# Optimization experiments

Hardware: AMD Instinct MI355X
Metric: run time of the kernel (lower is better)

The kernel has to match this reference:

```python
import jax, jax.numpy as jnp
from jax import lax
import numpy as np

GAMMA = 1.0
BIG = 1e10  # stand-in for +inf; exp(-BIG/gamma) underflows to 0 and keeps grads finite


def pairwise_sq_euclidean(A, B):
    # A: (B,T1,K), B: (B,T2,K) -> (B,T1,T2); 0.5*||a-b||^2 expanded to avoid (B,T1,T2,K)
    aa = 0.5 * jnp.sum(A * A, axis=-1)  # (B,T1)
    bb = 0.5 * jnp.sum(B * B, axis=-1)  # (B,T2)
    ab = jnp.einsum('bik,bjk->bij', A, B)
    return aa[:, :, None] + bb[:, None, :] - ab


def soft_dtw(C, gamma):
    # C: (B, m, n). Sequential DP: V[i,j] = C[i-1,j-1] + softmin_gamma(V[i,j-1], V[i-1,j-1], V[i-1,j])
    Bsz, m, n = C.shape
    dt = C.dtype
    big = jnp.asarray(BIG, dt)
    # row 0 of V: V[0,0]=0, V[0,j]=inf
    v0 = jnp.concatenate([jnp.zeros((Bsz, 1), dt), jnp.full((Bsz, n), big, dt)], axis=1)

    def row_step(v_prev, c_row):
        # v_prev: (B, n+1) = V[i-1, :]; c_row: (B, n) = C[:, i-1, :]
        def col_step(v_left, inp):
            c, v_diag, v_up = inp  # each (B,)
            prev = jnp.stack([v_left, v_diag, v_up], axis=-1)  # (B,3)
            minv = -gamma * jax.nn.logsumexp(-prev / gamma, axis=-1)
            v_new = c + minv
            return v_new, v_new

        xs = (c_row.T, v_prev[:, :-1].T, v_prev[:, 1:].T)  # (n, B) each
        _, vals = lax.scan(col_step, jnp.full((Bsz,), big, dt), xs)
        v_row = jnp.concatenate([jnp.full((Bsz, 1), big, dt), vals.T], axis=1)
        return v_row, None

    v_final, _ = lax.scan(row_step, v0, jnp.moveaxis(C, 1, 0))
    return v_final[:, -1]  # (B,)


def setup_inputs() -> dict:
    key = jax.random.key(0)
    k1, k2 = jax.random.split(key)
    X = jax.random.normal(k1, (512, 256, 64), dtype=jnp.float32)
    Y = jax.random.normal(k2, (512, 256, 64), dtype=jnp.float32)
    return {"X": X, "Y": Y}


def reference(X, Y):
    gamma = jnp.asarray(GAMMA, X.dtype)
    s_xy = soft_dtw(pairwise_sq_euclidean(X, Y), gamma)
    s_xx = soft_dtw(pairwise_sq_euclidean(X, X), gamma)
    s_yy = soft_dtw(pairwise_sq_euclidean(Y, Y), gamma)
    D = s_xy - 0.5 * s_xx - 0.5 * s_yy
    # normalize=False, reduction='mean'
    return jnp.mean(D)
```

## Files before the change

### kernel.cpp

```cpp
#include <hip/hip_runtime.h>

typedef float f4 __attribute__((ext_vector_type(4)));

#define BIGV 1e10f
#define LOG2E 1.44269504f
#define LN2 0.69314718f
#define RSTR 66

__device__ __forceinline__ float softmin3b(float a, float b, float c) {
  float m, d, M;
  asm("v_min3_f32 %0, %1, %2, %3" : "=v"(m) : "v"(a), "v"(b), "v"(c));
  asm("v_max3_f32 %0, %1, %2, %3" : "=v"(M) : "v"(a), "v"(b), "v"(c));
  asm("v_med3_f32 %0, %1, %2, %3" : "=v"(d) : "v"(a), "v"(b), "v"(c));
  float s = 1.0f + __builtin_amdgcn_exp2f(m - d) + __builtin_amdgcn_exp2f(m - M);
  return m - __log2f(s);
}

__device__ __forceinline__ float sumsq_fp8x4(unsigned int pk) {
  float d0 = __builtin_amdgcn_cvt_f32_fp8((int)pk, 0);
  float d1 = __builtin_amdgcn_cvt_f32_fp8((int)pk, 1);
  float d2 = __builtin_amdgcn_cvt_f32_fp8((int)pk, 2);
  float d3 = __builtin_amdgcn_cvt_f32_fp8((int)pk, 3);
  return (d0 * d0 + d1 * d1) + (d2 * d2 + d3 * d3);
}

__global__ __launch_bounds__(64)
void sdtw_c(const float* __restrict__ X, const float* __restrict__ Y,
            float* __restrict__ out) {
  const int p = blockIdx.x;
  const int type = p >> 9;
  const int b = p & 511;
  const float* Ap = (type == 2 ? Y : X) + (size_t)b * 256 * 64;
  const float* Bp = (type == 1 ? X : Y) + (size_t)b * 256 * 64;
  const float wgt = (type == 0) ? (LN2 / 512.0f) : (-LN2 / 1024.0f);

  __shared__ unsigned int ring[32 * RSTR];
  __shared__ unsigned int sB[4096];
  __shared__ _Float16 saa[256];
  __shared__ _Float16 sbb[256];

  const int t = threadIdx.x;
  const int hk = t >> 4, lr = t & 15;

  #pragma unroll 1
  for (int i = 0; i < 33; ++i) {
    int idx = i * 64 + t;
    if (idx < 32 * RSTR) ring[idx] = 0u;
  }

  {
    const float4* B4 = (const float4*)Bp;
    const int q = t & 15;
    #pragma unroll 1
    for (int it = 0; it < 64; ++it) {
      int pidx = it * 64 + t;
      int row = pidx >> 4;
      float4 v = B4[pidx];
      unsigned int pk = __builtin_amdgcn_cvt_pk_fp8_f32(v.x, v.y, 0, false);
      pk = __builtin_amdgcn_cvt_pk_fp8_f32(v.z, v.w, pk, true);
      sB[row * 16 + (q ^ ((row & 7) << 1))] = pk;
      float pr = sumsq_fp8x4(pk);
      pr += __shfl_xor(pr, 1);
      pr += __shfl_xor(pr, 2);
      pr += __shfl_xor(pr, 4);
      pr += __shfl_xor(pr, 8);
      if (q == 0) sbb[row] = (_Float16)(0.5f * LOG2E * pr);
    }
  }

  uint2 af[16][2];
  #pragma unroll
  for (int Rt = 0; Rt < 16; ++Rt) {
    float nrm = 0.f;
    #pragma unroll
    for (int kk = 0; kk < 2; ++kk) {
      const float4* src = (const float4*)(Ap + (Rt * 16 + lr) * 64 + kk * 32 + hk * 8);
      float4 x = src[0], y = src[1];
      unsigned int p0 = __builtin_amdgcn_cvt_pk_fp8_f32(x.x, x.y, 0, false);
      p0 = __builtin_amdgcn_cvt_pk_fp8_f32(x.z, x.w, p0, true);
      unsigned int p1 = __builtin_amdgcn_cvt_pk_fp8_f32(y.x, y.y, 0, false);
      p1 = __builtin_amdgcn_cvt_pk_fp8_f32(y.z, y.w, p1, true);
      af[Rt][kk] = make_uint2(p0, p1);
      nrm += sumsq_fp8x4(p0) + sumsq_fp8x4(p1);
    }
    nrm += __shfl_xor(nrm, 16);
    nrm += __shfl_xor(nrm, 32);
    if (hk == 0) saa[Rt * 16 + lr] = (_Float16)(0.5f * LOG2E * nrm);
  }

  float vL1 = BIGV, vL2 = BIGV, vL3 = BIGV, vL4 = BIGV;
  float dg = (t == 0) ? 0.0f : BIGV;

  #define PRODUCE_TILE(RT, CT)                                                     \
    {                                                                              \
      int n_ = (CT) * 16 + lr;                                                     \
      int sw_ = n_ & 7;                                                            \
      uint2 b0_ = *(const uint2*)&sB[n_ * 16 + 2 * (hk ^ sw_)];                    \
      uint2 b1_ = *(const uint2*)&sB[n_ * 16 + 2 * ((hk + 4) ^ sw_)];              \
      f4 acc_ = {0.f, 0.f, 0.f, 0.f};                                              \
      acc_ = __builtin_amdgcn_mfma_f32_16x16x32_fp8_fp8(                           \
               __builtin_bit_cast(long, af[RT][0]), __builtin_bit_cast(long, b0_), \
               acc_, 0, 0, 0);                                                     \
      acc_ = __builtin_amdgcn_mfma_f32_16x16x32_fp8_fp8(                           \
               __builtin_bit_cast(long, af[RT][1]), __builtin_bit_cast(long, b1_), \
               acc_, 0, 0, 0);                                                     \
      int r0_ = (RT) * 16 + hk * 4;                                                \
      float bbv_ = (float)sbb[n_];                                                 \
      float c0_ = fmaf(-LOG2E, acc_.x, (float)saa[r0_ + 0] + bbv_);                \
      float c1_ = fmaf(-LOG2E, acc_.y, (float)saa[r0_ + 1] + bbv_);                \
      float c2_ = fmaf(-LOG2E, acc_.z, (float)saa[r0_ + 2] + bbv_);                \
      float c3_ = fmaf(-LOG2E, acc_.w, (float)saa[r0_ + 3] + bbv_);                \
      int pk_ = __builtin_amdgcn_cvt_pk_fp8_f32(c0_, c1_, 0, false);               \
      pk_ = __builtin_amdgcn_cvt_pk_fp8_f32(c2_, c3_, pk_, true);                  \
      int tr_ = 4 * (RT) + hk;                                                     \
      int s1_ = n_ + tr_;                                                          \
      ring[(s1_ & 31) * RSTR + tr_] = (unsigned int)pk_;                           \
    }

  #define DP_STEP(CW)                                                              \
    {                                                                              \
      float up1 = __shfl_up(vL4, 1);                                               \
      if (t == 0) up1 = BIGV;                                                      \
      float c0 = __builtin_amdgcn_cvt_f32_fp8((int)(CW), 0);                       \
      float c1 = __builtin_amdgcn_cvt_f32_fp8((int)(CW), 1);                       \
      float c2 = __builtin_amdgcn_cvt_f32_fp8((int)(CW), 2);                       \
      float c3 = __builtin_amdgcn_cvt_f32_fp8((int)(CW), 3);                       \
      float v1 = c0 + softmin3b(vL1, dg, up1);                                     \
      float v2 = c1 + softmin3b(vL2, vL1, v1);                                     \
      float v3 = c2 + softmin3b(vL3, vL2, v2);                                     \
      float v4 = c3 + softmin3b(vL4, vL3, v3);                                     \
      vL1 = v1; vL2 = v2; vL3 = v3; vL4 = v4; dg = up1;                            \
    }

  PRODUCE_TILE(0, 0)

  #pragma unroll 1
  for (int KB = 0; KB < 19; ++KB) {
    #pragma unroll
    for (int r = 0; r < 4; ++r) {
      const int k = 4 * KB + r;
      unsigned int w0 = ring[((4 * k + 0) & 31) * RSTR + t];
      unsigned int w1 = ring[((4 * k + 1) & 31) * RSTR + t];
      unsigned int w2 = ring[((4 * k + 2) & 31) * RSTR + t];
      unsigned int w3 = ring[((4 * k + 3) & 31) * RSTR + t];
      if (k < 75) {
        const int KBp = KB + (r == 3 ? 1 : 0);
        #pragma unroll
        for (int dlt = 0; dlt < 4; ++dlt) {
          int Ct = KBp - dlt;
          if (Ct >= 0 && Ct <= 15) {
            PRODUCE_TILE(((r + 1) & 3) + 4 * dlt, Ct)
          }
        }
      }
      DP_STEP(w0)
      DP_STEP(w1)
      DP_STEP(w2)
      DP_STEP(w3)
    }
  }

  #pragma unroll 1
  for (int u = 0; u < 15; ++u) {
    unsigned int cw = ring[((304 + u) & 31) * RSTR + t];
    DP_STEP(cw)
  }

  if (t == 63) atomicAdd(out, wgt * vL4);
}

extern "C" void kernel_launch(void* const* d_in, const int* in_sizes, int n_in,
                              void* d_out, int out_size, void* d_ws, size_t ws_size,
                              hipStream_t stream) {
  const float* X = (const float*)d_in[0];
  const float* Y = (const float*)d_in[1];
  float* out = (float*)d_out;
  hipMemsetAsync(out, 0, sizeof(float) * out_size, stream);
  sdtw_c<<<1536, 64, 0, stream>>>(X, Y, out);
}
```

Measured before the change: 160.9 us.

## Warp-specialize producer/consumer waves and recast soft-DTW DP in mantissa-exponent form

```diff
diff --git a/kernel.cpp b/kernel.cpp
--- a/kernel.cpp
+++ b/kernel.cpp
@@ -2,19 +2,10 @@
 
 typedef float f4 __attribute__((ext_vector_type(4)));
 
-#define BIGV 1e10f
 #define LOG2E 1.44269504f
 #define LN2 0.69314718f
-#define RSTR 66
-
-__device__ __forceinline__ float softmin3b(float a, float b, float c) {
-  float m, d, M;
-  asm("v_min3_f32 %0, %1, %2, %3" : "=v"(m) : "v"(a), "v"(b), "v"(c));
-  asm("v_max3_f32 %0, %1, %2, %3" : "=v"(M) : "v"(a), "v"(b), "v"(c));
-  asm("v_med3_f32 %0, %1, %2, %3" : "=v"(d) : "v"(a), "v"(b), "v"(c));
-  float s = 1.0f + __builtin_amdgcn_exp2f(m - d) + __builtin_amdgcn_exp2f(m - M);
-  return m - __log2f(s);
-}
+#define DEADD (1 << 28)
+#define RS2 66
 
 __device__ __forceinline__ float sumsq_fp8x4(unsigned int pk) {
   float d0 = __builtin_amdgcn_cvt_f32_fp8((int)pk, 0);
@@ -24,9 +15,20 @@
   return (d0 * d0 + d1 * d1) + (d2 * d2 + d3 * d3);
 }
 
-__global__ __launch_bounds__(64)
-void sdtw_c(const float* __restrict__ X, const float* __restrict__ Y,
-            float* __restrict__ out) {
+__device__ __forceinline__ void cellf(float& Eo, int& don,
+                                      float EL, int dL, float ED, int dD,
+                                      float EU, int dU, float m, int ci126) {
+  int ref = min(min(dL, dD), dU);
+  float S = ldexpf(EL, ref - dL) + ldexpf(ED, ref - dD) + ldexpf(EU, ref - dU);
+  float v = m * S;
+  unsigned int u = __builtin_bit_cast(unsigned int, v);
+  Eo = __builtin_bit_cast(float, (u & 0x007FFFFFu) | 0x3F000000u);
+  don = (ref + ci126) - (int)(u >> 23);
+}
+
+__global__ __launch_bounds__(128)
+void sdtw_ws(const float* __restrict__ X, const float* __restrict__ Y,
+             float* __restrict__ out) {
   const int p = blockIdx.x;
   const int type = p >> 9;
   const int b = p & 511;
@@ -34,26 +36,29 @@
   const float* Bp = (type == 1 ? X : Y) + (size_t)b * 256 * 64;
   const float wgt = (type == 0) ? (LN2 / 512.0f) : (-LN2 / 1024.0f);
 
-  __shared__ unsigned int ring[32 * RSTR];
+  __shared__ uint2 ring[32 * RS2];
   __shared__ unsigned int sB[4096];
   __shared__ _Float16 saa[256];
   __shared__ _Float16 sbb[256];
 
-  const int t = threadIdx.x;
-  const int hk = t >> 4, lr = t & 15;
+  const int tid = threadIdx.x;
+  const int wv = tid >> 6;
+  const int lane = tid & 63;
+  const int hk = lane >> 4, lr = lane & 15;
+  const int bpaddr = ((lane + 63) & 63) << 2;
 
   #pragma unroll 1
-  for (int i = 0; i < 33; ++i) {
-    int idx = i * 64 + t;
-    if (idx < 32 * RSTR) ring[idx] = 0u;
+  for (int i = 0; i < 17; ++i) {
+    int idx = i * 128 + tid;
+    if (idx < 32 * RS2) ring[idx] = make_uint2(0u, 0u);
   }
 
   {
     const float4* B4 = (const float4*)Bp;
-    const int q = t & 15;
+    const int q = tid & 15;
     #pragma unroll 1
-    for (int it = 0; it < 64; ++it) {
-      int pidx = it * 64 + t;
+    for (int it = 0; it < 32; ++it) {
+      int pidx = it * 128 + tid;
       int row = pidx >> 4;
       float4 v = B4[pidx];
       unsigned int pk = __builtin_amdgcn_cvt_pk_fp8_f32(v.x, v.y, 0, false);
@@ -69,27 +74,27 @@
   }
 
   uint2 af[16][2];
-  #pragma unroll
-  for (int Rt = 0; Rt < 16; ++Rt) {
-    float nrm = 0.f;
+  if (wv == 0) {
     #pragma unroll
-    for (int kk = 0; kk < 2; ++kk) {
-      const float4* src = (const float4*)(Ap + (Rt * 16 + lr) * 64 + kk * 32 + hk * 8);
-      float4 x = src[0], y = src[1];
-      unsigned int p0 = __builtin_amdgcn_cvt_pk_fp8_f32(x.x, x.y, 0, false);
-      p0 = __builtin_amdgcn_cvt_pk_fp8_f32(x.z, x.w, p0, true);
-      unsigned int p1 = __builtin_amdgcn_cvt_pk_fp8_f32(y.x, y.y, 0, false);
-      p1 = __builtin_amdgcn_cvt_pk_fp8_f32(y.z, y.w, p1, true);
-      af[Rt][kk] = make_uint2(p0, p1);
-      nrm += sumsq_fp8x4(p0) + sumsq_fp8x4(p1);
-    }
-    nrm += __shfl_xor(nrm, 16);
-    nrm += __shfl_xor(nrm, 32);
-    if (hk == 0) saa[Rt * 16 + lr] = (_Float16)(0.5f * LOG2E * nrm);
-  }
-
-  float vL1 = BIGV, vL2 = BIGV, vL3 = BIGV, vL4 = BIGV;
-  float dg = (t == 0) ? 0.0f : BIGV;
+    for (int Rt = 0; Rt < 16; ++Rt) {
+      float nrm = 0.f;
+      #pragma unroll
+      for (int kk = 0; kk < 2; ++kk) {
+        const float4* src = (const float4*)(Ap + (Rt * 16 + lr) * 64 + kk * 32 + hk * 8);
+        float4 x = src[0], y = src[1];
+        unsigned int p0 = __builtin_amdgcn_cvt_pk_fp8_f32(x.x, x.y, 0, false);
+        p0 = __builtin_amdgcn_cvt_pk_fp8_f32(x.z, x.w, p0, true);
+        unsigned int p1 = __builtin_amdgcn_cvt_pk_fp8_f32(y.x, y.y, 0, false);
+        p1 = __builtin_amdgcn_cvt_pk_fp8_f32(y.z, y.w, p1, true);
+        af[Rt][kk] = make_uint2(p0, p1);
+        nrm += sumsq_fp8x4(p0) + sumsq_fp8x4(p1);
+      }
+      nrm += __shfl_xor(nrm, 16);
+      nrm += __shfl_xor(nrm, 32);
+      if (hk == 0) saa[Rt * 16 + lr] = (_Float16)(0.5f * LOG2E * nrm);
+    }
+  }
+  __syncthreads();
 
   #define PRODUCE_TILE(RT, CT)                                                     \
     {                                                                              \
@@ -106,67 +111,114 @@
                acc_, 0, 0, 0);                                                     \
       int r0_ = (RT) * 16 + hk * 4;                                                \
       float bbv_ = (float)sbb[n_];                                                 \
-      float c0_ = fmaf(-LOG2E, acc_.x, (float)saa[r0_ + 0] + bbv_);                \
-      float c1_ = fmaf(-LOG2E, acc_.y, (float)saa[r0_ + 1] + bbv_);                \
-      float c2_ = fmaf(-LOG2E, acc_.z, (float)saa[r0_ + 2] + bbv_);                \
-      float c3_ = fmaf(-LOG2E, acc_.w, (float)saa[r0_ + 3] + bbv_);                \
-      int pk_ = __builtin_amdgcn_cvt_pk_fp8_f32(c0_, c1_, 0, false);               \
-      pk_ = __builtin_amdgcn_cvt_pk_fp8_f32(c2_, c3_, pk_, true);                  \
+      float c0_ = fminf(fmaxf(fmaf(-LOG2E, acc_.x, (float)saa[r0_ + 0] + bbv_), 0.f), 254.0f); \
+      float c1_ = fminf(fmaxf(fmaf(-LOG2E, acc_.y, (float)saa[r0_ + 1] + bbv_), 0.f), 254.0f); \
+      float c2_ = fminf(fmaxf(fmaf(-LOG2E, acc_.z, (float)saa[r0_ + 2] + bbv_), 0.f), 254.0f); \
+      float c3_ = fminf(fmaxf(fmaf(-LOG2E, acc_.w, (float)saa[r0_ + 3] + bbv_), 0.f), 254.0f); \
+      float f0_ = truncf(c0_), f1_ = truncf(c1_), f2_ = truncf(c2_), f3_ = truncf(c3_); \
+      float x0_ = c0_ - f0_, x1_ = c1_ - f1_, x2_ = c2_ - f2_, x3_ = c3_ - f3_;    \
+      float m0_ = fmaf(x0_, fmaf(x0_, 0.17157f, -0.67157f), 1.0f);                 \
+      float m1_ = fmaf(x1_, fmaf(x1_, 0.17157f, -0.67157f), 1.0f);                 \
+      float m2_ = fmaf(x2_, fmaf(x2_, 0.17157f, -0.67157f), 1.0f);                 \
+      float m3_ = fmaf(x3_, fmaf(x3_, 0.17157f, -0.67157f), 1.0f);                 \
+      int pkm_ = __builtin_amdgcn_cvt_pk_fp8_f32(m0_, m1_, 0, false);              \
+      pkm_ = __builtin_amdgcn_cvt_pk_fp8_f32(m2_, m3_, pkm_, true);                \
+      unsigned int pkc_ = (unsigned int)f0_ | ((unsigned int)f1_ << 8)             \
+                        | ((unsigned int)f2_ << 16) | ((unsigned int)f3_ << 24);   \
       int tr_ = 4 * (RT) + hk;                                                     \
       int s1_ = n_ + tr_;                                                          \
-      ring[(s1_ & 31) * RSTR + tr_] = (unsigned int)pk_;                           \
-    }
-
-  #define DP_STEP(CW)                                                              \
+      ring[(s1_ & 31) * RS2 + tr_] = make_uint2((unsigned int)pkm_, pkc_);         \
+    }
+
+  float E1 = 0.f, E2 = 0.f, E3 = 0.f, E4 = 0.f;
+  int d1 = DEADD, d2 = DEADD, d3 = DEADD, d4 = DEADD;
+  float dgE = (lane == 0) ? 1.0f : 0.f;
+  int dgd = (lane == 0) ? 0 : DEADD;
+
+  #define DP_STEP(W)                                                               \
     {                                                                              \
-      float up1 = __shfl_up(vL4, 1);                                               \
-      if (t == 0) up1 = BIGV;                                                      \
-      float c0 = __builtin_amdgcn_cvt_f32_fp8((int)(CW), 0);                       \
-      float c1 = __builtin_amdgcn_cvt_f32_fp8((int)(CW), 1);                       \
-      float c2 = __builtin_amdgcn_cvt_f32_fp8((int)(CW), 2);                       \
-      float c3 = __builtin_amdgcn_cvt_f32_fp8((int)(CW), 3);                       \
-      float v1 = c0 + softmin3b(vL1, dg, up1);                                     \
-      float v2 = c1 + softmin3b(vL2, vL1, v1);                                     \
-      float v3 = c2 + softmin3b(vL3, vL2, v2);                                     \
-      float v4 = c3 + softmin3b(vL4, vL3, v3);                                     \
-      vL1 = v1; vL2 = v2; vL3 = v3; vL4 = v4; dg = up1;                            \
-    }
-
-  PRODUCE_TILE(0, 0)
+      float upE = __builtin_bit_cast(float,                                        \
+          __builtin_amdgcn_ds_bpermute(bpaddr, __builtin_bit_cast(int, E4)));      \
+      int upd = __builtin_amdgcn_ds_bpermute(bpaddr, d4);                          \
+      if (lane == 0) { upE = 0.f; upd = DEADD; }                                   \
+      float m0 = __builtin_amdgcn_cvt_f32_fp8((int)(W).x, 0);                      \
+      float m1 = __builtin_amdgcn_cvt_f32_fp8((int)(W).x, 1);                      \
+      float m2 = __builtin_amdgcn_cvt_f32_fp8((int)(W).x, 2);                      \
+      float m3 = __builtin_amdgcn_cvt_f32_fp8((int)(W).x, 3);                      \
+      int c0 = (int)((W).y & 255u) + 126;                                          \
+      int c1 = (int)(((W).y >> 8) & 255u) + 126;                                   \
+      int c2 = (int)(((W).y >> 16) & 255u) + 126;                                  \
+      int c3 = (int)((W).y >> 24) + 126;                                           \
+      float v1E, v2E, v3E, v4E; int v1d, v2d, v3d, v4d;                            \
+      cellf(v1E, v1d, E1, d1, dgE, dgd, upE, upd, m0, c0);                         \
+      cellf(v2E, v2d, E2, d2, E1, d1, v1E, v1d, m1, c1);                           \
+      cellf(v3E, v3d, E3, d3, E2, d2, v2E, v2d, m2, c2);                           \
+      cellf(v4E, v4d, E4, d4, E3, d3, v3E, v3d, m3, c3);                           \
+      E1 = v1E; d1 = v1d; E2 = v2E; d2 = v2d;                                      \
+      E3 = v3E; d3 = v3d; E4 = v4E; d4 = v4d;                                      \
+      dgE = upE; dgd = upd;                                                        \
+    }
+
+  #define CONSUME8(L0)                                                             \
+    {                                                                              \
+      uint2 w0 = ring[(((L0) + 0) & 31) * RS2 + lane];                             \
+      uint2 w1 = ring[(((L0) + 1) & 31) * RS2 + lane];                             \
+      uint2 w2 = ring[(((L0) + 2) & 31) * RS2 + lane];                             \
+      uint2 w3 = ring[(((L0) + 3) & 31) * RS2 + lane];                             \
+      uint2 w4 = ring[(((L0) + 4) & 31) * RS2 + lane];                             \
+      uint2 w5 = ring[(((L0) + 5) & 31) * RS2 + lane];                             \
+      uint2 w6 = ring[(((L0) + 6) & 31) * RS2 + lane];                             \
+      uint2 w7 = ring[(((L0) + 7) & 31) * RS2 + lane];                             \
+      DP_STEP(w0) DP_STEP(w1) DP_STEP(w2) DP_STEP(w3)                              \
+      DP_STEP(w4) DP_STEP(w5) DP_STEP(w6) DP_STEP(w7)                              \
+    }
+
+  if (wv == 0) {
+    PRODUCE_TILE(0, 0)
+    PRODUCE_TILE(1, 0)
+  }
+  __syncthreads();
 
   #pragma unroll 1
-  for (int KB = 0; KB < 19; ++KB) {
-    #pragma unroll
-    for (int r = 0; r < 4; ++r) {
-      const int k = 4 * KB + r;
-      unsigned int w0 = ring[((4 * k + 0) & 31) * RSTR + t];
-      unsigned int w1 = ring[((4 * k + 1) & 31) * RSTR + t];
-      unsigned int w2 = ring[((4 * k + 2) & 31) * RSTR + t];
-      unsigned int w3 = ring[((4 * k + 3) & 31) * RSTR + t];
-      if (k < 75) {
-        const int KBp = KB + (r == 3 ? 1 : 0);
+  for (int hh = 0; hh < 19; ++hh) {
+    if (wv == 0) {
+      #pragma unroll
+      for (int dlt = 0; dlt < 4; ++dlt) {
+        int Ct = hh - dlt;
+        if (Ct >= 0 && Ct <= 15) {
+          PRODUCE_TILE(2 + 4 * dlt, Ct)
+          PRODUCE_TILE(3 + 4 * dlt, Ct)
+        }
+      }
+    } else {
+      CONSUME8(16 * hh)
+    }
+    __syncthreads();
+    if (wv == 0) {
+      if (hh < 18) {
         #pragma unroll
         for (int dlt = 0; dlt < 4; ++dlt) {
-          int Ct = KBp - dlt;
+          int Ct = hh + 1 - dlt;
           if (Ct >= 0 && Ct <= 15) {
-            PRODUCE_TILE(((r + 1) & 3) + 4 * dlt, Ct)
+            PRODUCE_TILE(0 + 4 * dlt, Ct)
+            PRODUCE_TILE(1 + 4 * dlt, Ct)
           }
         }
       }
-      DP_STEP(w0)
-      DP_STEP(w1)
-      DP_STEP(w2)
-      DP_STEP(w3)
-    }
-  }
-
-  #pragma unroll 1
-  for (int u = 0; u < 15; ++u) {
-    unsigned int cw = ring[((304 + u) & 31) * RSTR + t];
-    DP_STEP(cw)
-  }
-
-  if (t == 63) atomicAdd(out, wgt * vL4);
+    } else {
+      CONSUME8(16 * hh + 8)
+    }
+    __syncthreads();
+  }
+
+  if (wv == 1) {
+    #pragma unroll 1
+    for (int u = 0; u < 15; ++u) {
+      uint2 cw = ring[((304 + u) & 31) * RS2 + lane];
+      DP_STEP(cw)
+    }
+    if (lane == 63) atomicAdd(out, wgt * ((float)d4 - __log2f(E4)));
+  }
 }
 
 extern "C" void kernel_launch(void* const* d_in, const int* in_sizes, int n_in,
@@ -176,5 +228,5 @@
   const float* Y = (const float*)d_in[1];
   float* out = (float*)d_out;
   hipMemsetAsync(out, 0, sizeof(float) * out_size, stream);
-  sdtw_c<<<1536, 64, 0, stream>>>(X, Y, out);
-}
+  sdtw_ws<<<1536, 128, 0, stream>>>(X, Y, out);
+}
```

Result: slower. 167.2 us (+3.9%).
